# Performance work log

Measured on AMD Instinct MI355X. Metric: run time of the kernel, lower is better.

## Reference

```python
import jax, jax.numpy as jnp
import numpy as np

EPS = 1e-5  # BatchNorm2d default eps


def conv1x1(x, w, b):
    # x: (B,C,H,W), w: (O,C), b: (O,)
    return jnp.einsum('bchw,oc->bohw', x, w) + b[None, :, None, None]


def bn_relu(x, g, beta, m, v):
    # inference-mode BatchNorm2d followed by ReLU; per-channel params (C,)
    s = g * jax.lax.rsqrt(v + EPS)
    return jax.nn.relu(x * s[None, :, None, None] + (beta - m * s)[None, :, None, None])


def setup_inputs() -> dict:
    key = jax.random.key(0)
    B, Cin, H, W = 4, 512, 64, 64
    Ck, Cv, Cout = 256, 256, 512
    ks = jax.random.split(key, 16)
    WSCALE = 0.03  # keep activations / softmax logits in a sane range

    def branch_params(k, first_in):
        k = jax.random.split(k, 8)
        return dict(
            w1=jax.random.normal(k[0], (Ck, first_in), jnp.float32) * WSCALE,
            b1=jax.random.normal(k[1], (Ck,), jnp.float32) * 0.01,
            g1=jnp.ones((Ck,), jnp.float32),
            beta1=jnp.zeros((Ck,), jnp.float32),
            m1=jax.random.normal(k[2], (Ck,), jnp.float32) * 0.05,
            v1=jax.random.uniform(k[3], (Ck,), jnp.float32, 0.5, 1.5),
            w2=jax.random.normal(k[4], (Ck, Ck), jnp.float32) * WSCALE,
            b2=jax.random.normal(k[5], (Ck,), jnp.float32) * 0.01,
            g2=jnp.ones((Ck,), jnp.float32),
            beta2=jnp.zeros((Ck,), jnp.float32),
            m2=jax.random.normal(k[6], (Ck,), jnp.float32) * 0.05,
            v2=jax.random.uniform(k[7], (Ck,), jnp.float32, 0.5, 1.5),
        )

    kb = branch_params(ks[1], Cin)
    qb = branch_params(ks[2], Cin)
    d = {'x': jax.random.normal(ks[0], (B, Cin, H, W), jnp.float32)}
    for name, p in (('k', kb), ('q', qb)):
        for pk, pv in p.items():
            d[f'{name}_{pk}'] = pv
    d['v_w'] = jax.random.normal(ks[3], (Cv, Cin), jnp.float32) * WSCALE
    d['v_b'] = jax.random.normal(ks[4], (Cv,), jnp.float32) * 0.01
    d['o_w'] = jax.random.normal(ks[5], (Cout, Cv), jnp.float32) * WSCALE
    d['o_b'] = jax.random.normal(ks[6], (Cout,), jnp.float32) * 0.01
    return d


def reference(x,
              k_w1, k_b1, k_g1, k_beta1, k_m1, k_v1,
              k_w2, k_b2, k_g2, k_beta2, k_m2, k_v2,
              q_w1, q_b1, q_g1, q_beta1, q_m1, q_v1,
              q_w2, q_b2, q_g2, q_beta2, q_m2, q_v2,
              v_w, v_b, o_w, o_b):
    B, C, H, W = x.shape
    Ck = k_w1.shape[0]
    Cv = v_w.shape[0]
    N = H * W

    def branch(w1, b1, g1, be1, m1, v1, w2, b2, g2, be2, m2, v2):
        h = bn_relu(conv1x1(x, w1, b1), g1, be1, m1, v1)
        return bn_relu(conv1x1(h, w2, b2), g2, be2, m2, v2)

    value = conv1x1(x, v_w, v_b).reshape(B, Cv, N)                       # (B,Cv,N)
    query = branch(q_w1, q_b1, q_g1, q_beta1, q_m1, q_v1,
                   q_w2, q_b2, q_g2, q_beta2, q_m2, q_v2).reshape(B, Ck, N)
    keyf = branch(k_w1, k_b1, k_g1, k_beta1, k_m1, k_v1,
                  k_w2, k_b2, k_g2, k_beta2, k_m2, k_v2).reshape(B, Ck, N)

    # sim_map[b,n,m] = <query[:,n], key[:,m]> * Ck^-0.5, softmax over m
    sim = jnp.einsum('bcn,bcm->bnm', query, keyf) * (Ck ** -0.5)         # (B,N,N)
    attn = jax.nn.softmax(sim, axis=-1)
    ctx = jnp.einsum('bnm,bcm->bcn', attn, value).reshape(B, Cv, H, W)   # (B,Cv,H,W)
    return conv1x1(ctx, o_w, o_b)                                        # (B,Cout,H,W)
```

## Files before the change

kernel.cpp:

```cpp
#include <hip/hip_runtime.h>
#include <hip/hip_bf16.h>

typedef unsigned short u16;
typedef __attribute__((ext_vector_type(8))) unsigned short u16x8;
typedef __attribute__((ext_vector_type(4))) unsigned short u16x4;
typedef __attribute__((ext_vector_type(4))) float f32x4;

#define MFMA16(a,b,c) __builtin_amdgcn_mfma_f32_16x16x32_bf16((a),(b),(c),0,0,0)
#define LOG2E 1.44269504f

static __device__ __forceinline__ float b2f(u16 b) {
  unsigned int u = ((unsigned int)b) << 16;
  float f;
  __builtin_memcpy(&f, &u, 4);
  return f;
}
static __device__ __forceinline__ u16 f2b(float x) {
  __hip_bfloat16 h = __float2bfloat16(x);
  u16 u;
  __builtin_memcpy(&u, &h, 2);
  return u;
}
static __device__ __forceinline__ u16x8 ld8(const u16* p) {
  u16x8 v;
  __builtin_memcpy(&v, p, 16);
  return v;
}
static __device__ __forceinline__ void st8(u16* p, u16x8 v) {
  __builtin_memcpy(p, &v, 16);
}
#define MEMFENCE() __asm__ __volatile__("" ::: "memory")
static __device__ __forceinline__ bool is_fp32(const unsigned int* probe) {
  return probe[0] == 0x3F800000u;
}

typedef __attribute__((address_space(1))) const void gas_void;
typedef __attribute__((address_space(3))) void las_void;
static __device__ __forceinline__ void gload16(const u16* g, u16* l) {
  __builtin_amdgcn_global_load_lds((gas_void*)g, (las_void*)l, 16, 0, 0);
}

static __device__ __forceinline__ uint3 xcd_swz() {
  unsigned nx = gridDim.x, ny = gridDim.y;
  unsigned nwg = nx * ny * gridDim.z;
  unsigned lin = (blockIdx.z * ny + blockIdx.y) * nx + blockIdx.x;
  unsigned wg = (lin & 7u) * (nwg >> 3) + (lin >> 3);
  uint3 r;
  r.x = wg % nx;
  unsigned t = wg / nx;
  r.y = t % ny;
  r.z = t / ny;
  return r;
}

struct ParamPack {
  const void* p[28];
  int sz[28];
  int off[28];
};
__global__ __launch_bounds__(256)
void convert_params(ParamPack pk, u16* __restrict__ dst,
                    const unsigned int* __restrict__ probe) {
  const int b = blockIdx.x;
  const int n = pk.sz[b], o = pk.off[b];
  if (is_fp32(probe)) {
    const float* s = (const float*)pk.p[b];
    for (int i = threadIdx.x * 4; i + 3 < n; i += 1024) {
      float4 v;
      __builtin_memcpy(&v, s + i, 16);
      u16x4 w = { f2b(v.x), f2b(v.y), f2b(v.z), f2b(v.w) };
      __builtin_memcpy(dst + o + i, &w, 8);
    }
    for (int t = (n & ~3) + threadIdx.x; t < n; t += 256) dst[o + t] = f2b(s[t]);
  } else {
    const u16* s = (const u16*)pk.p[b];
    for (int i = threadIdx.x * 8; i + 7 < n; i += 2048) st8(dst + o + i, ld8(s + i));
    for (int t = (n & ~7) + threadIdx.x; t < n; t += 256) dst[o + t] = s[t];
  }
}

__global__ __launch_bounds__(256)
void transpose_cn(const void* __restrict__ xv, u16* __restrict__ xt,
                  const unsigned int* __restrict__ probe) {
  __shared__ u16 tile[64][65];
  const int b = blockIdx.z;
  const int n0 = blockIdx.x * 64, c0 = blockIdx.y * 64;
  const int tn = threadIdx.x & 63, tr = threadIdx.x >> 6;
  if (is_fp32(probe)) {
    const float* xb = (const float*)xv + (size_t)b * 512 * 4096;
    #pragma unroll
    for (int i = tr; i < 64; i += 4)
      tile[i][tn] = f2b(xb[(size_t)(c0 + i) * 4096 + n0 + tn]);
  } else {
    const u16* xb = (const u16*)xv + (size_t)b * 512 * 4096;
    #pragma unroll
    for (int i = tr; i < 64; i += 4)
      tile[i][tn] = xb[(size_t)(c0 + i) * 4096 + n0 + tn];
  }
  __syncthreads();
  u16* xtb = xt + (size_t)b * 4096 * 512;
  #pragma unroll
  for (int i = tr; i < 64; i += 4)
    xtb[(size_t)(n0 + i) * 512 + c0 + tn] = tile[tn][i];
}

static __device__ __forceinline__ void gemm_core(
    const u16* __restrict__ A, const u16* __restrict__ Bb, int K,
    int nb, int mb0, u16* __restrict__ lds, f32x4 acc[2][4])
{
  const int tid = threadIdx.x;
  const int lane = tid & 63, wave = tid >> 6;
  const int quad = lane >> 4, l15 = lane & 15;
  const int mb1 = mb0 + 64;

  const u16* a0 = A + (size_t)(mb0 + l15) * K + quad * 8;
  const u16* a1 = A + (size_t)(mb1 + l15) * K + quad * 8;

  const int srow = tid >> 3;
  const int scol = ((tid & 7) ^ (srow & 7)) * 8;
  const u16* bsrc = Bb + (size_t)(nb + srow) * K + scol;
  const int swz = (l15 & 7) * 8;

  #pragma unroll
  for (int i = 0; i < 2; ++i)
    #pragma unroll
    for (int t = 0; t < 4; ++t)
      acc[i][t] = (f32x4){0.f, 0.f, 0.f, 0.f};

  {
    u16* d = lds + wave * 512;
    gload16(bsrc, d);
    gload16(bsrc + (size_t)32 * K, d + 2048);
  }
  u16x8 afA0 = ld8(a0), afA1 = ld8(a0 + 32);
  u16x8 afB0 = ld8(a1), afB1 = ld8(a1 + 32);
  u16x8 anA0 = afA0, anA1 = afA1, anB0 = afB0, anB1 = afB1;

  int cur = 0;
  for (int k = 0; k < K; k += 64) {
    __syncthreads();
    if (k + 64 < K) {
      u16* d = lds + (cur ^ 1) * 4096 + wave * 512;
      gload16(bsrc + k + 64, d);
      gload16(bsrc + (size_t)32 * K + k + 64, d + 2048);
      anA0 = ld8(a0 + k + 64); anA1 = ld8(a0 + k + 96);
      anB0 = ld8(a1 + k + 64); anB1 = ld8(a1 + k + 96);
    }
    const u16* bl = lds + cur * 4096;
    #pragma unroll
    for (int t = 0; t < 4; ++t) {
      const u16* br = bl + (size_t)(t * 16 + l15) * 64;
      u16x8 bf0 = ld8(br + ((quad * 8) ^ swz));
      acc[0][t] = MFMA16(afA0, bf0, acc[0][t]);
      acc[1][t] = MFMA16(afB0, bf0, acc[1][t]);
      u16x8 bf1 = ld8(br + (((4 + quad) * 8) ^ swz));
      acc[0][t] = MFMA16(afA1, bf1, acc[0][t]);
      acc[1][t] = MFMA16(afB1, bf1, acc[1][t]);
    }
    afA0 = anA0; afA1 = anA1; afB0 = anB0; afB1 = anB1;
    cur ^= 1;
  }
}

static __device__ __forceinline__ void epi_bn_T(
    f32x4 acc[2][4], u16* __restrict__ ob, int M, int nb, int mb0,
    const u16* __restrict__ bias, const u16* __restrict__ g,
    const u16* __restrict__ be, const u16* __restrict__ mu,
    const u16* __restrict__ vr)
{
  const int lane = threadIdx.x & 63;
  const int quad = lane >> 4, l15 = lane & 15;
  #pragma unroll
  for (int i = 0; i < 2; ++i) {
    const int mb = mb0 + i * 64;
    float sc[4], sh[4];
    #pragma unroll
    for (int r = 0; r < 4; ++r) {
      int o = mb + quad * 4 + r;
      float s = b2f(g[o]) * rsqrtf(b2f(vr[o]) + 1e-5f);
      sc[r] = s;
      sh[r] = b2f(be[o]) - b2f(mu[o]) * s + b2f(bias[o]) * s;
    }
    #pragma unroll
    for (int t = 0; t < 4; ++t) {
      int n = nb + t * 16 + l15;
      float y0 = fmaxf(acc[i][t][0] * sc[0] + sh[0], 0.f);
      float y1 = fmaxf(acc[i][t][1] * sc[1] + sh[1], 0.f);
      float y2 = fmaxf(acc[i][t][2] * sc[2] + sh[2], 0.f);
      float y3 = fmaxf(acc[i][t][3] * sc[3] + sh[3], 0.f);
      u16x4 pk = { f2b(y0), f2b(y1), f2b(y2), f2b(y3) };
      __builtin_memcpy(&ob[(size_t)n * M + mb + quad * 4], &pk, 8);
    }
  }
}

static __device__ __forceinline__ void epi_plain_N(
    f32x4 acc[2][4], u16* __restrict__ ob, int nb, int mb0,
    const u16* __restrict__ bias)
{
  const int N = 4096;
  const int lane = threadIdx.x & 63;
  const int quad = lane >> 4, l15 = lane & 15;
  #pragma unroll
  for (int i = 0; i < 2; ++i) {
    const int mb = mb0 + i * 64;
    float sh[4];
    #pragma unroll
    for (int r = 0; r < 4; ++r) sh[r] = b2f(bias[mb + quad * 4 + r]);
    #pragma unroll
    for (int t = 0; t < 4; ++t) {
      int n = nb + t * 16 + l15;
      #pragma unroll
      for (int r = 0; r < 4; ++r)
        ob[(size_t)(mb + quad * 4 + r) * N + n] = f2b(acc[i][t][r] + sh[r]);
    }
  }
}

__global__ __launch_bounds__(256)
void gemm_f1(const u16* __restrict__ xt, u16* __restrict__ vv,
             u16* __restrict__ h1q, u16* __restrict__ h1k,
             const u16* __restrict__ vw, const u16* __restrict__ vb,
             const u16* __restrict__ qw, const u16* __restrict__ qb,
             const u16* __restrict__ qg, const u16* __restrict__ qbe,
             const u16* __restrict__ qm, const u16* __restrict__ qv,
             const u16* __restrict__ kw, const u16* __restrict__ kb,
             const u16* __restrict__ kg, const u16* __restrict__ kbe,
             const u16* __restrict__ km, const u16* __restrict__ kv)
{
  __shared__ u16 blds[2 * 64 * 64];
  const uint3 wg = xcd_swz();
  const int b = wg.z;
  const int sel = wg.y >> 1;
  const int wave = threadIdx.x >> 6;
  const int nb = wg.x * 64;
  const int mb0 = (wg.y & 1) * 128 + wave * 16;

  const u16* Bb = xt + (size_t)b * 4096 * 512;
  const u16* A = (sel == 0) ? vw : (sel == 1) ? qw : kw;

  f32x4 acc[2][4];
  gemm_core(A, Bb, 512, nb, mb0, blds, acc);

  if (sel == 0) {
    epi_plain_N(acc, vv + (size_t)b * 256 * 4096, nb, mb0, vb);
  } else if (sel == 1) {
    epi_bn_T(acc, h1q + (size_t)b * 4096 * 256, 256, nb, mb0,
             qb, qg, qbe, qm, qv);
  } else {
    epi_bn_T(acc, h1k + (size_t)b * 4096 * 256, 256, nb, mb0,
             kb, kg, kbe, km, kv);
  }
}

__global__ __launch_bounds__(256)
void gemm_f2(const u16* __restrict__ h1q, const u16* __restrict__ h1k,
             u16* __restrict__ qt, u16* __restrict__ kt,
             const u16* __restrict__ qw, const u16* __restrict__ qb,
             const u16* __restrict__ qg, const u16* __restrict__ qbe,
             const u16* __restrict__ qm, const u16* __restrict__ qv,
             const u16* __restrict__ kw, const u16* __restrict__ kb,
             const u16* __restrict__ kg, const u16* __restrict__ kbe,
             const u16* __restrict__ km, const u16* __restrict__ kv)
{
  __shared__ u16 blds[2 * 64 * 64];
  const uint3 wg = xcd_swz();
  const int b = wg.z >> 1;
  const int br = wg.z & 1;
  const int wave = threadIdx.x >> 6;
  const int nb = wg.x * 64;
  const int mb0 = wg.y * 128 + wave * 16;

  const u16* Bb = (br ? h1k : h1q) + (size_t)b * 4096 * 256;
  const u16* A = br ? kw : qw;

  f32x4 acc[2][4];
  gemm_core(A, Bb, 256, nb, mb0, blds, acc);

  u16* ob = (br ? kt : qt) + (size_t)b * 4096 * 256;
  if (br) epi_bn_T(acc, ob, 256, nb, mb0, kb, kg, kbe, km, kv);
  else    epi_bn_T(acc, ob, 256, nb, mb0, qb, qg, qbe, qm, qv);
}

__global__ __launch_bounds__(256)
void gemm_nt(const u16* __restrict__ A, const u16* __restrict__ Bt,
             void* __restrict__ outv, int M, int K,
             const u16* __restrict__ bias,
             const unsigned int* __restrict__ oprobe)
{
  const int N = 4096;
  __shared__ u16 blds[2 * 64 * 64];
  const uint3 wg = xcd_swz();
  const int b = wg.z;
  const int lane = threadIdx.x & 63, wave = threadIdx.x >> 6;
  const int quad = lane >> 4, l15 = lane & 15;
  const int nb = wg.x * 64;
  const int mb0 = wg.y * 128 + wave * 16;

  const u16* Bb = Bt + (size_t)b * N * K;
  f32x4 acc[2][4];
  gemm_core(A, Bb, K, nb, mb0, blds, acc);

  if (oprobe != nullptr && is_fp32(oprobe)) {
    float* ob = (float*)outv + (size_t)b * M * N;
    #pragma unroll
    for (int i = 0; i < 2; ++i) {
      const int mb = mb0 + i * 64;
      float sh[4];
      #pragma unroll
      for (int r = 0; r < 4; ++r) sh[r] = b2f(bias[mb + quad * 4 + r]);
      #pragma unroll
      for (int t = 0; t < 4; ++t) {
        int n = nb + t * 16 + l15;
        #pragma unroll
        for (int r = 0; r < 4; ++r)
          ob[(size_t)(mb + quad * 4 + r) * N + n] = acc[i][t][r] + sh[r];
      }
    }
  } else {
    u16* ob = (u16*)outv + (size_t)b * M * N;
    #pragma unroll
    for (int i = 0; i < 2; ++i) {
      const int mb = mb0 + i * 64;
      float sh[4];
      #pragma unroll
      for (int r = 0; r < 4; ++r) sh[r] = b2f(bias[mb + quad * 4 + r]);
      #pragma unroll
      for (int t = 0; t < 4; ++t) {
        int n = nb + t * 16 + l15;
        #pragma unroll
        for (int r = 0; r < 4; ++r)
          ob[(size_t)(mb + quad * 4 + r) * N + n] = f2b(acc[i][t][r] + sh[r]);
      }
    }
  }
}

__global__ __launch_bounds__(256, 2)
void attn_k5(const u16* __restrict__ Qt, const u16* __restrict__ Kt,
             const u16* __restrict__ V, u16* __restrict__ part,
             float* __restrict__ scales)
{
  const int N = 4096, D = 256, SPLIT = 2048;
  __shared__ u16 kt_lds[2][32][256];
  __shared__ u16 v_lds[2][256][32];
  __shared__ u16 p_lds[4][16][40];

  const uint3 wg = xcd_swz();
  const int b = wg.y;
  const int sp = wg.z;
  const int tid = threadIdx.x;
  const int lane = tid & 63, wave = tid >> 6;
  const int quad = lane >> 4, l15 = lane & 15;
  const int q0 = wg.x * 64 + wave * 16;
  const int k0 = sp * SPLIT;

  const u16* Qb = Qt + (size_t)b * N * D;
  const u16* Kb = Kt + (size_t)b * N * D;
  const u16* Vb = V + (size_t)b * D * N;

  const int krow = tid >> 5;
  const int kcol = ((tid & 31) ^ krow) * 8;
  const int vswz = (tid >> 3) & 7;

  auto stage = [&](int bi, int m0) {
    u16* kd = (bi ? &kt_lds[1][0][0] : &kt_lds[0][0][0]) + wave * 512;
    u16* vd = (bi ? &v_lds[1][0][0] : &v_lds[0][0][0]) + wave * 512;
    #pragma unroll
    for (int j = 0; j < 4; ++j) {
      gload16(Kb + (size_t)(m0 + j * 8 + krow) * D + kcol, kd + j * 2048);
      int gc = (j * 256 + tid) ^ vswz;
      gload16(Vb + (size_t)(gc >> 2) * N + m0 + (gc & 3) * 8, vd + j * 2048);
    }
  };

  u16x8 qf[8];
  #pragma unroll
  for (int ks = 0; ks < 8; ++ks)
    qf[ks] = ld8(&Qb[(size_t)(q0 + l15) * D + ks * 32 + quad * 8]);

  u16x8 ones;
  #pragma unroll
  for (int i = 0; i < 8; ++i) ones[i] = 0x3F80;

  f32x4 oacc[16];
  #pragma unroll
  for (int ct = 0; ct < 16; ++ct) oacc[ct] = (f32x4){0.f, 0.f, 0.f, 0.f};
  f32x4 lacc = (f32x4){0.f, 0.f, 0.f, 0.f};
  float mrow[4] = {-1e30f, -1e30f, -1e30f, -1e30f};

  stage(0, k0);
  int cur = 0;
  for (int it = 0; it < SPLIT / 32; ++it) {
    __syncthreads();
    if (it + 1 < SPLIT / 32) stage(cur ^ 1, k0 + (it + 1) * 32);

    const u16* kl = cur ? &kt_lds[1][0][0] : &kt_lds[0][0][0];
    const u16* vl = cur ? &v_lds[1][0][0] : &v_lds[0][0][0];

    f32x4 s0 = (f32x4){0.f, 0.f, 0.f, 0.f};
    f32x4 s1 = (f32x4){0.f, 0.f, 0.f, 0.f};
    __builtin_amdgcn_s_setprio(1);
    #pragma unroll
    for (int ks = 0; ks < 8; ++ks) {
      int c0 = ((ks * 4 + quad) * 8) ^ ((l15 & 7) * 8);
      u16x8 bk0 = ld8(kl + (size_t)l15 * 256 + c0);
      u16x8 bk1 = ld8(kl + (size_t)(16 + l15) * 256 + c0);
      s0 = MFMA16(qf[ks], bk0, s0);
      s1 = MFMA16(qf[ks], bk1, s1);
    }
    __builtin_amdgcn_s_setprio(0);

    float a[4], c[4];
    int bad = 0;
    #pragma unroll
    for (int r = 0; r < 4; ++r) {
      a[r] = s0[r] * 0.0625f;
      c[r] = s1[r] * 0.0625f;
      bad |= (fmaxf(a[r], c[r]) - mrow[r] > 8.f) ? 1 : 0;
    }
    if (__builtin_expect(__any(bad), 0)) {
      float alpha[4];
      #pragma unroll
      for (int r = 0; r < 4; ++r) {
        float mx = fmaxf(a[r], c[r]);
        mx = fmaxf(mx, __shfl_xor(mx, 1));
        mx = fmaxf(mx, __shfl_xor(mx, 2));
        mx = fmaxf(mx, __shfl_xor(mx, 4));
        mx = fmaxf(mx, __shfl_xor(mx, 8));
        float mnew = fmaxf(mrow[r], mx);
        alpha[r] = exp2f((mrow[r] - mnew) * LOG2E);
        mrow[r] = mnew;
      }
      #pragma unroll
      for (int ct = 0; ct < 16; ++ct) {
        oacc[ct][0] *= alpha[0];
        oacc[ct][1] *= alpha[1];
        oacc[ct][2] *= alpha[2];
        oacc[ct][3] *= alpha[3];
      }
      lacc[0] *= alpha[0];
      lacc[1] *= alpha[1];
      lacc[2] *= alpha[2];
      lacc[3] *= alpha[3];
    }
    #pragma unroll
    for (int r = 0; r < 4; ++r) {
      float p0 = exp2f((a[r] - mrow[r]) * LOG2E);
      float p1 = exp2f((c[r] - mrow[r]) * LOG2E);
      p_lds[wave][quad * 4 + r][l15] = f2b(p0);
      p_lds[wave][quad * 4 + r][16 + l15] = f2b(p1);
    }
    MEMFENCE();

    u16x8 pf = ld8(&p_lds[wave][l15][quad * 8]);

    __builtin_amdgcn_s_setprio(1);
    #pragma unroll
    for (int ct = 0; ct < 16; ++ct) {
      int gc = ct * 64 + l15 * 4 + quad;
      u16x8 vf = ld8(vl + (size_t)(gc ^ (l15 >> 1)) * 8);
      oacc[ct] = MFMA16(pf, vf, oacc[ct]);
    }
    lacc = MFMA16(pf, ones, lacc);
    __builtin_amdgcn_s_setprio(0);
    MEMFENCE();
    cur ^= 1;
  }

  float inv[4];
  #pragma unroll
  for (int r = 0; r < 4; ++r) inv[r] = 1.f / lacc[r];
  u16* Pb = part + (size_t)sp * 4194304 + (size_t)b * N * D;
  #pragma unroll
  for (int ct = 0; ct < 16; ++ct) {
    #pragma unroll
    for (int r = 0; r < 4; ++r) {
      Pb[(size_t)(q0 + quad * 4 + r) * D + ct * 16 + l15] =
          f2b(oacc[ct][r] * inv[r]);
    }
  }
  if (l15 == 0) {
    #pragma unroll
    for (int r = 0; r < 4; ++r) {
      size_t row = (size_t)q0 + quad * 4 + r;
      size_t o = (((size_t)sp * 4 + b) * 4096 + row) * 2;
      scales[o + 0] = mrow[r];
      scales[o + 1] = lacc[r];
    }
  }
}

__global__ __launch_bounds__(256)
void attn_merge(u16* __restrict__ part, const float* __restrict__ scales) {
  const int b = blockIdx.y;
  const int n = blockIdx.x * 4 + (threadIdx.x >> 6);
  const int c = (threadIdx.x & 63) * 4;
  const size_t stride = (size_t)4194304;
  const size_t row = ((size_t)b * 4096 + n) * 256;
  const size_t s0 = (((size_t)0 * 4 + b) * 4096 + n) * 2;
  const size_t s1 = (((size_t)1 * 4 + b) * 4096 + n) * 2;
  float m0 = scales[s0], l0 = scales[s0 + 1];
  float m1 = scales[s1], l1 = scales[s1 + 1];
  float m = fmaxf(m0, m1);
  float w0 = exp2f((m0 - m) * LOG2E) * l0;
  float w1 = exp2f((m1 - m) * LOG2E) * l1;
  float inv = 1.f / (w0 + w1);
  w0 *= inv; w1 *= inv;
  u16x4 p0, p1;
  __builtin_memcpy(&p0, &part[row + c], 8);
  __builtin_memcpy(&p1, &part[stride + row + c], 8);
  u16x4 o;
  #pragma unroll
  for (int i = 0; i < 4; ++i)
    o[i] = f2b(b2f(p0[i]) * w0 + b2f(p1[i]) * w1);
  __builtin_memcpy(&part[row + c], &o, 8);
}

extern "C" void kernel_launch(void* const* d_in, const int* in_sizes, int n_in,
                              void* d_out, int out_size, void* d_ws, size_t ws_size,
                              hipStream_t stream) {
  (void)n_in; (void)out_size;
  if (ws_size < (size_t)43789824) return;

  const unsigned int* probe = (const unsigned int*)d_in[3];

  ParamPack pk;
  int off = 0;
  for (int i = 0; i < 28; ++i) {
    pk.p[i] = d_in[i + 1];
    pk.sz[i] = in_sizes[i + 1];
    pk.off[i] = off;
    off += in_sizes[i + 1];
  }

  u16* ws  = (u16*)d_ws;
  u16* xt  = ws;
  u16* h1q = ws + 8388608;
  u16* h1k = ws + 12582912;
  u16* vv  = ws + 16777216;
  u16* qt  = ws;
  u16* kt  = ws + 4194304;
  u16* part = ws + 8388608;
  u16* ot  = part;
  u16* P   = ws + 20971520;
  float* scales = (float*)(ws + 21632768);

  const u16 *ck_w1 = P + pk.off[0],  *ck_b1 = P + pk.off[1],
            *ck_g1 = P + pk.off[2],  *ck_be1 = P + pk.off[3],
            *ck_m1 = P + pk.off[4],  *ck_v1 = P + pk.off[5],
            *ck_w2 = P + pk.off[6],  *ck_b2 = P + pk.off[7],
            *ck_g2 = P + pk.off[8],  *ck_be2 = P + pk.off[9],
            *ck_m2 = P + pk.off[10], *ck_v2 = P + pk.off[11],
            *cq_w1 = P + pk.off[12], *cq_b1 = P + pk.off[13],
            *cq_g1 = P + pk.off[14], *cq_be1 = P + pk.off[15],
            *cq_m1 = P + pk.off[16], *cq_v1 = P + pk.off[17],
            *cq_w2 = P + pk.off[18], *cq_b2 = P + pk.off[19],
            *cq_g2 = P + pk.off[20], *cq_be2 = P + pk.off[21],
            *cq_m2 = P + pk.off[22], *cq_v2 = P + pk.off[23],
            *cv_w  = P + pk.off[24], *cv_b  = P + pk.off[25],
            *co_w  = P + pk.off[26], *co_b  = P + pk.off[27];

  convert_params<<<28, 256, 0, stream>>>(pk, P, probe);
  transpose_cn<<<dim3(64, 8, 4), 256, 0, stream>>>(d_in[0], xt, probe);

  gemm_f1<<<dim3(64, 6, 4), 256, 0, stream>>>(xt, vv, h1q, h1k,
      cv_w, cv_b,
      cq_w1, cq_b1, cq_g1, cq_be1, cq_m1, cq_v1,
      ck_w1, ck_b1, ck_g1, ck_be1, ck_m1, ck_v1);
  gemm_f2<<<dim3(64, 2, 8), 256, 0, stream>>>(h1q, h1k, qt, kt,
      cq_w2, cq_b2, cq_g2, cq_be2, cq_m2, cq_v2,
      ck_w2, ck_b2, ck_g2, ck_be2, ck_m2, ck_v2);
  attn_k5<<<dim3(64, 4, 2), 256, 0, stream>>>(qt, kt, vv, part, scales);
  attn_merge<<<dim3(1024, 4), 256, 0, stream>>>(part, scales);
  gemm_nt<<<dim3(64, 4, 4), 256, 0, stream>>>(co_w, ot, d_out, 512, 256,
      co_b, probe);
}
```

Measured before the change: 353.8 us.

## Load V fragments directly from global into registers, bypassing LDS staging

The attention kernel now skips staging V tiles in shared memory. Each wave issues 16 per-lane 16-byte global loads straight into MFMA B-operand registers at the start of each iteration, and waits on them with explicit vmcnt before the PV MFMAs. This removes the V LDS buffers, their LDS reads and write traffic, and frees LDS for occupancy. In exchange it raises register pressure by 64 VGPRs, makes each wave load V redundantly (four times per workgroup), and exposes global latency inside the loop with only the QK^T compute to hide it.

```diff
diff --git a/kernel.cpp b/kernel.cpp
--- a/kernel.cpp
+++ b/kernel.cpp
@@ -343,7 +343,6 @@
 {
   const int N = 4096, D = 256, SPLIT = 2048;
   __shared__ u16 kt_lds[2][32][256];
-  __shared__ u16 v_lds[2][256][32];
   __shared__ u16 p_lds[4][16][40];
 
   const uint3 wg = xcd_swz();
@@ -361,18 +360,20 @@
 
   const int krow = tid >> 5;
   const int kcol = ((tid & 31) ^ krow) * 8;
-  const int vswz = (tid >> 3) & 7;
 
   auto stage = [&](int bi, int m0) {
     u16* kd = (bi ? &kt_lds[1][0][0] : &kt_lds[0][0][0]) + wave * 512;
-    u16* vd = (bi ? &v_lds[1][0][0] : &v_lds[0][0][0]) + wave * 512;
-    #pragma unroll
-    for (int j = 0; j < 4; ++j) {
+    #pragma unroll
+    for (int j = 0; j < 4; ++j)
       gload16(Kb + (size_t)(m0 + j * 8 + krow) * D + kcol, kd + j * 2048);
-      int gc = (j * 256 + tid) ^ vswz;
-      gload16(Vb + (size_t)(gc >> 2) * N + m0 + (gc & 3) * 8, vd + j * 2048);
-    }
   };
+
+  unsigned voff[16];
+  #pragma unroll
+  for (int ct = 0; ct < 16; ++ct)
+    voff[ct] = (unsigned)(((ct * 16 + l15) * N + quad * 8) * 2);
+  unsigned long long sv =
+      (unsigned long long)(uintptr_t)Vb + (unsigned long long)k0 * 2;
 
   u16x8 qf[8];
   #pragma unroll
@@ -392,11 +393,19 @@
   stage(0, k0);
   int cur = 0;
   for (int it = 0; it < SPLIT / 32; ++it) {
+    const int notlast = (it + 1 < SPLIT / 32);
     __syncthreads();
-    if (it + 1 < SPLIT / 32) stage(cur ^ 1, k0 + (it + 1) * 32);
+
+    u16x8 vfr[16];
+    #pragma unroll
+    for (int ct = 0; ct < 16; ++ct)
+      asm volatile("global_load_dwordx4 %0, %1, %2"
+                   : "=v"(vfr[ct]) : "v"(voff[ct]), "s"(sv));
+    __builtin_amdgcn_sched_barrier(0);
+
+    if (notlast) stage(cur ^ 1, k0 + (it + 1) * 32);
 
     const u16* kl = cur ? &kt_lds[1][0][0] : &kt_lds[0][0][0];
-    const u16* vl = cur ? &v_lds[1][0][0] : &v_lds[0][0][0];
 
     f32x4 s0 = (f32x4){0.f, 0.f, 0.f, 0.f};
     f32x4 s1 = (f32x4){0.f, 0.f, 0.f, 0.f};
@@ -455,16 +464,18 @@
 
     u16x8 pf = ld8(&p_lds[wave][l15][quad * 8]);
 
+    if (notlast) asm volatile("s_waitcnt vmcnt(4)" ::: "memory");
+    else         asm volatile("s_waitcnt vmcnt(0)" ::: "memory");
+    __builtin_amdgcn_sched_barrier(0);
+
     __builtin_amdgcn_s_setprio(1);
     #pragma unroll
-    for (int ct = 0; ct < 16; ++ct) {
-      int gc = ct * 64 + l15 * 4 + quad;
-      u16x8 vf = ld8(vl + (size_t)(gc ^ (l15 >> 1)) * 8);
-      oacc[ct] = MFMA16(pf, vf, oacc[ct]);
-    }
+    for (int ct = 0; ct < 16; ++ct)
+      oacc[ct] = MFMA16(pf, vfr[ct], oacc[ct]);
     lacc = MFMA16(pf, ones, lacc);
     __builtin_amdgcn_s_setprio(0);
     MEMFENCE();
+    sv += 64;
     cur ^= 1;
   }
 
```

Measured after the change: 535.0 us. 1.51x slower.
